# Kernel optimization log

Hardware: AMD Instinct MI355X
Metric: run time of the kernel (lower is better)

The kernel has to match this reference:

```python
import jax, jax.numpy as jnp
import numpy as np

N = 10000
E = 160000
D = 512
EPS = 1e-5


def _lin_params(key, out_d, in_d, bias=True):
    k1, k2 = jax.random.split(key)
    s = 1.0 / np.sqrt(in_d)
    W = jax.random.uniform(k1, (out_d, in_d), jnp.float32, -s, s)
    if bias:
        b = jax.random.uniform(k2, (out_d,), jnp.float32, -s, s)
        return W, b
    return (W,)


def setup_inputs() -> dict:
    key = jax.random.key(0)
    ks = jax.random.split(key, 16)
    inp = {
        "x": jax.random.normal(ks[0], (N, D), jnp.float32),
        "edge_index": jax.random.randint(ks[1], (2, E), 0, N, jnp.int64),
    }
    ki = 2
    for l in range(3):
        Wp, bp = _lin_params(ks[ki], D, D); ki += 1
        Wl, bl = _lin_params(ks[ki], D, D); ki += 1
        (Wr,) = _lin_params(ks[ki], D, D, bias=False); ki += 1
        inp[f"Wp{l}"] = Wp; inp[f"bp{l}"] = bp
        inp[f"Wl{l}"] = Wl; inp[f"bl{l}"] = bl
        inp[f"Wr{l}"] = Wr
        if l < 2:  # ReLU+LayerNorm between convs
            inp[f"g{l}"] = jnp.ones((D,), jnp.float32)
            inp[f"be{l}"] = jnp.zeros((D,), jnp.float32)
    return inp


def _sage_conv(x, src, dst, Wp, bp, Wl, bl, Wr):
    # PyG SAGEConv with project=True: project+ReLU messages, mean-aggregate, lin_l + lin_r(root)
    h = jax.nn.relu(x @ Wp.T + bp)                      # [N, D] projected messages
    agg = jax.ops.segment_sum(h[src], dst, num_segments=N)   # gather + scatter-add
    cnt = jax.ops.segment_sum(jnp.ones((src.shape[0],), x.dtype), dst, num_segments=N)
    agg = agg / jnp.maximum(cnt, 1.0)[:, None]          # mean over incoming edges
    return agg @ Wl.T + bl + x @ Wr.T


def _relu_ln(x, g, b):
    x = jax.nn.relu(x)
    mu = jnp.mean(x, axis=-1, keepdims=True)
    var = jnp.mean(jnp.square(x - mu), axis=-1, keepdims=True)
    return (x - mu) * jax.lax.rsqrt(var + EPS) * g + b


def reference(x, edge_index,
              Wp0, bp0, Wl0, bl0, Wr0, g0, be0,
              Wp1, bp1, Wl1, bl1, Wr1, g1, be1,
              Wp2, bp2, Wl2, bl2, Wr2):
    src, dst = edge_index[0], edge_index[1]
    x = _sage_conv(x, src, dst, Wp0, bp0, Wl0, bl0, Wr0)
    x = _relu_ln(x, g0, be0)
    x = _sage_conv(x, src, dst, Wp1, bp1, Wl1, bl1, Wr1)
    x = _relu_ln(x, g1, be1)
    x = _sage_conv(x, src, dst, Wp2, bp2, Wl2, bl2, Wr2)
    return x
```

## Files before the change

kernel.cpp:

```cpp
#include <hip/hip_runtime.h>
#include <cstdint>

#define D 512
#define TM 128
#define TN 64
#define BK 32
#define CAP 64

typedef unsigned short u16;
typedef __bf16 bf16x8 __attribute__((ext_vector_type(8)));
typedef float f32x4 __attribute__((ext_vector_type(4)));

__device__ __forceinline__ float bf2f(u16 u) {
    unsigned int x = ((unsigned int)u) << 16;
    return __builtin_bit_cast(float, x);
}
__device__ __forceinline__ u16 f2bf(float f) {
    unsigned int x = __builtin_bit_cast(unsigned int, f);
    x += 0x7fffu + ((x >> 16) & 1u);
    return (u16)(x >> 16);
}
__device__ __forceinline__ float loadf(const void* p, int i, bool bf) {
    return bf ? bf2f(((const u16*)p)[i]) : ((const float*)p)[i];
}
__device__ __forceinline__ void gload16(const u16* g, u16* l) {
    __builtin_amdgcn_global_load_lds(
        (const __attribute__((address_space(1))) void*)(uintptr_t)g,
        (__attribute__((address_space(3))) void*)(unsigned int)(uintptr_t)l,
        16, 0, 0);
}
__device__ __forceinline__ void drain_vm() {
    asm volatile("s_waitcnt vmcnt(0)" ::: "memory");
}
__device__ __forceinline__ bool is_bf16(const u16* xraw) {
    int lane = threadIdx.x & 63;
    u16 u = xraw[2 * lane];
    int e = (u >> 7) & 0xFF;
    unsigned long long b = __ballot(e >= 110 && e <= 129);
    return __popcll(b) >= 32;
}
__device__ __forceinline__ bool is_i64(const int* eraw) {
    int lane = threadIdx.x & 63;
    unsigned long long b = __ballot(eraw[2 * lane + 1] == 0);
    return __popcll(b) >= 32;
}

struct PrepArgs {
    const u16* xraw; const int* eraw;
    const void* W[9];
    const void* V[10];
    u16* xb; u16* Wb; float* vecf;
    int* cnt; u16* bucket;
    int M, E;
};

__global__ __launch_bounds__(256) void prep(PrepArgs a)
{
    const bool bf  = is_bf16(a.xraw);
    const bool i64 = is_i64(a.eraw);
    const int gt = blockIdx.x * 256 + threadIdx.x;
    const int gs = gridDim.x * 256;

    const int nx = a.M * D / 8;
    for (int i = gt; i < nx; i += gs) {
        if (bf) {
            *(uint4*)(a.xb + i * 8) = *(const uint4*)(a.xraw + i * 8);
        } else {
            const float* f = (const float*)a.xraw + i * 8;
            float4 p = *(const float4*)f, q = *(const float4*)(f + 4);
            u16 r[8] = {f2bf(p.x), f2bf(p.y), f2bf(p.z), f2bf(p.w),
                        f2bf(q.x), f2bf(q.y), f2bf(q.z), f2bf(q.w)};
            *(uint4*)(a.xb + i * 8) = *(uint4*)r;
        }
    }

    for (int i = gt; i < 9 * 32768; i += gs) {
        int m = i >> 15, j = i & 32767;
        const void* gsrc = nullptr;
        if (m == 3 || m == 5) gsrc = a.V[2];
        else if (m == 6 || m == 8) gsrc = a.V[6];
        const void* src = a.W[m];
        int c0 = (j * 8) & 511;
        float v[8];
        if (bf) {
            const u16* s = (const u16*)src + j * 8;
#pragma unroll
            for (int e = 0; e < 8; e++) v[e] = bf2f(s[e]);
        } else {
            const float* s = (const float*)src + j * 8;
#pragma unroll
            for (int e = 0; e < 8; e++) v[e] = s[e];
        }
        if (gsrc) {
#pragma unroll
            for (int e = 0; e < 8; e++) v[e] *= loadf(gsrc, c0 + e, bf);
        }
        u16 r[8];
#pragma unroll
        for (int e = 0; e < 8; e++) r[e] = f2bf(v[e]);
        *(uint4*)(a.Wb + (size_t)m * D * D + j * 8) = *(uint4*)r;
    }

    for (int e = gt; e < 10 * 512; e += gs) {
        int t = e >> 9, n = e & 511;
        float outv;
        if (t == 0)      outv = loadf(a.V[0], n, bf);
        else if (t == 1) outv = loadf(a.V[1], n, bf);
        else {
            int q = t - 2;
            const int wi[8] = {3, 3, 5, 5, 6, 6, 8, 8};
            const void* wraw = a.W[wi[q]];
            const void* dotv = (q < 4) ? ((q & 1) ? a.V[3] : a.V[2])
                                       : ((q & 1) ? a.V[7] : a.V[6]);
            float acc = 0.f;
            if (bf) {
                const u16* wr = (const u16*)wraw + (size_t)n * 512;
                for (int k = 0; k < 512; k++) acc += bf2f(wr[k]) * loadf(dotv, k, bf);
            } else {
                const float* wr = (const float*)wraw + (size_t)n * 512;
                for (int k = 0; k < 512; k++) acc += wr[k] * loadf(dotv, k, bf);
            }
            if (q & 1) {
                const void* braw = (q == 1) ? a.V[4] : (q == 3) ? a.V[5]
                                 : (q == 5) ? a.V[8] : a.V[9];
                acc += loadf(braw, n, bf);
            }
            outv = acc;
        }
        a.vecf[t * 512 + n] = outv;
    }

    for (int e2 = gt; e2 < a.E; e2 += gs) {
        int s, d;
        if (i64) { s = a.eraw[2 * e2]; d = a.eraw[2 * (a.E + e2)]; }
        else     { s = a.eraw[e2];     d = a.eraw[a.E + e2]; }
        s = min(max(s, 0), a.M - 1);
        d = min(max(d, 0), a.M - 1);
        int p = atomicAdd(&a.cnt[d], 1);
        if (p < CAP) a.bucket[(size_t)d * CAP + p] = (u16)s;
    }
}

template <bool LNIN>
__global__ __launch_bounds__(256) void gemm1k(
    const u16* __restrict__ A, const u16* __restrict__ W,
    const float* __restrict__ bias, const float* __restrict__ svec,
    const float* __restrict__ mu, const float* __restrict__ m2,
    u16* __restrict__ hout, int M)
{
    __shared__ __align__(16) u16 sA[2][TM * BK];
    __shared__ __align__(16) u16 sB[2][TN * BK];

    const int t    = threadIdx.x;
    const int m0   = blockIdx.x * TM;
    const int n0   = blockIdx.y * TN;
    const int wave = t >> 6, lane = t & 63;
    const int wm   = wave >> 1, wn = wave & 1;
    const int lrow = lane & 15, quad = lane >> 4;

    float rstd[4][4], nmu[4][4];
    if (LNIN) {
#pragma unroll
        for (int mi = 0; mi < 4; mi++)
#pragma unroll
            for (int r = 0; r < 4; r++) {
                int row = min(m0 + wm * 64 + mi * 16 + quad * 4 + r, M - 1);
                float mean = mu[row] * (1.f / 512.f);
                float var  = m2[row] * (1.f / 512.f) - mean * mean;
                float rs   = rsqrtf(fmaxf(var, 0.f) + 1e-5f);
                rstd[mi][r] = rs;
                nmu[mi][r]  = -mean * rs;
            }
    }

    f32x4 acc[4][2];
#pragma unroll
    for (int i = 0; i < 4; i++)
#pragma unroll
        for (int j = 0; j < 2; j++)
#pragma unroll
            for (int r = 0; r < 4; r++) acc[i][j][r] = 0.f;

    const int cA    = (t & 3) * 8;
    const int rowA0 = min(m0 + (t >> 2),      M - 1);
    const int rowA1 = min(m0 + 64 + (t >> 2), M - 1);
    const int rowB  = n0 + (t >> 2);
    const u16* gA0 = A + (size_t)rowA0 * D + cA;
    const u16* gA1 = A + (size_t)rowA1 * D + cA;
    const u16* gB  = W + (size_t)rowB  * D + cA;

    gload16(gA0, &sA[0][(size_t)t * 8]);
    gload16(gA1, &sA[0][(size_t)(t + 256) * 8]);
    gload16(gB,  &sB[0][(size_t)t * 8]);

#pragma unroll 1
    for (int k0 = 0; k0 < D; k0 += BK) {
        const int it  = k0 >> 5;
        const int cur = it & 1, nxt = cur ^ 1;
        drain_vm();
        __syncthreads();
        const int k1 = k0 + BK;
        if (k1 < D) {
            gload16(gA0 + k1, &sA[nxt][(size_t)t * 8]);
            gload16(gA1 + k1, &sA[nxt][(size_t)(t + 256) * 8]);
            gload16(gB  + k1, &sB[nxt][(size_t)t * 8]);
        }
        bf16x8 af[4], bfr[2];
#pragma unroll
        for (int mi = 0; mi < 4; mi++)
            af[mi] = *(const bf16x8*)&sA[cur][(wm * 64 + mi * 16 + lrow) * BK + quad * 8];
#pragma unroll
        for (int ni = 0; ni < 2; ni++)
            bfr[ni] = *(const bf16x8*)&sB[cur][(wn * 32 + ni * 16 + lrow) * BK + quad * 8];
#pragma unroll
        for (int mi = 0; mi < 4; mi++)
#pragma unroll
            for (int ni = 0; ni < 2; ni++)
                acc[mi][ni] = __builtin_amdgcn_mfma_f32_16x16x32_bf16(
                    af[mi], bfr[ni], acc[mi][ni], 0, 0, 0);
    }

#pragma unroll
    for (int ni = 0; ni < 2; ni++) {
        int col = n0 + wn * 32 + ni * 16 + lrow;
        float bv = bias[col];
        float sv = LNIN ? svec[col] : 0.f;
#pragma unroll
        for (int mi = 0; mi < 4; mi++) {
            int row0 = m0 + wm * 64 + mi * 16 + quad * 4;
#pragma unroll
            for (int r = 0; r < 4; r++) {
                int row = row0 + r;
                if (row < M) {
                    float v = LNIN ? rstd[mi][r] * acc[mi][ni][r] + nmu[mi][r] * sv + bv
                                   : acc[mi][ni][r] + bv;
                    hout[(size_t)row * D + col] = f2bf(fmaxf(v, 0.f));
                }
            }
        }
    }
}

template <bool LNIN, bool STATS, bool FINAL>
__global__ __launch_bounds__(256) void gemm2k(
    const u16* __restrict__ A0, const u16* __restrict__ W0,
    const u16* __restrict__ A1, const u16* __restrict__ W1,
    const float* __restrict__ bias, const float* __restrict__ s2vec,
    const float* __restrict__ mu_in, const float* __restrict__ m2_in,
    float* __restrict__ mu_out, float* __restrict__ m2_out,
    void* __restrict__ out, const u16* __restrict__ xraw, int M)
{
    __shared__ __align__(16) u16 sA[2][TM * BK];
    __shared__ __align__(16) u16 sB[2][TN * BK];

    const int t    = threadIdx.x;
    const int m0   = blockIdx.x * TM;
    const int n0   = blockIdx.y * TN;
    const int wave = t >> 6, lane = t & 63;
    const int wm   = wave >> 1, wn = wave & 1;
    const int lrow = lane & 15, quad = lane >> 4;

    const bool out_bf16 = FINAL ? is_bf16(xraw) : true;

    float rstd[4][4], nmu[4][4], inv[4][4];
    if (LNIN) {
#pragma unroll
        for (int mi = 0; mi < 4; mi++)
#pragma unroll
            for (int r = 0; r < 4; r++) {
                int row = min(m0 + wm * 64 + mi * 16 + quad * 4 + r, M - 1);
                float mean = mu_in[row] * (1.f / 512.f);
                float var  = m2_in[row] * (1.f / 512.f) - mean * mean;
                float s    = sqrtf(fmaxf(var, 0.f) + 1e-5f);
                float rs   = 1.f / s;
                rstd[mi][r] = rs;
                inv[mi][r]  = s;
                nmu[mi][r]  = -mean * rs;
            }
    }

    f32x4 acc[4][2];
#pragma unroll
    for (int i = 0; i < 4; i++)
#pragma unroll
        for (int j = 0; j < 2; j++)
#pragma unroll
            for (int r = 0; r < 4; r++) acc[i][j][r] = 0.f;

    const int cA    = (t & 3) * 8;
    const int rowA0 = min(m0 + (t >> 2),      M - 1);
    const int rowA1 = min(m0 + 64 + (t >> 2), M - 1);
    const int rowB  = n0 + (t >> 2);

    gload16(A0 + (size_t)rowA0 * D + cA, &sA[0][(size_t)t * 8]);
    gload16(A0 + (size_t)rowA1 * D + cA, &sA[0][(size_t)(t + 256) * 8]);
    gload16(W0 + (size_t)rowB  * D + cA, &sB[0][(size_t)t * 8]);

#pragma unroll 1
    for (int kk = 0; kk < 2 * D; kk += BK) {
        const int it  = kk >> 5;
        const int cur = it & 1, nxt = cur ^ 1;
        drain_vm();
        __syncthreads();
        const int kn = kk + BK;
        if (kn < 2 * D) {
            const u16* A = (kn >= D) ? A1 : A0;
            const u16* W = (kn >= D) ? W1 : W0;
            const int k = kn & (D - 1);
            gload16(A + (size_t)rowA0 * D + k + cA, &sA[nxt][(size_t)t * 8]);
            gload16(A + (size_t)rowA1 * D + k + cA, &sA[nxt][(size_t)(t + 256) * 8]);
            gload16(W + (size_t)rowB  * D + k + cA, &sB[nxt][(size_t)t * 8]);
        }
        if (LNIN && kk == D) {
#pragma unroll
            for (int mi = 0; mi < 4; mi++)
#pragma unroll
                for (int ni = 0; ni < 2; ni++)
#pragma unroll
                    for (int r = 0; r < 4; r++) acc[mi][ni][r] *= inv[mi][r];
        }
        bf16x8 af[4], bfr[2];
#pragma unroll
        for (int mi = 0; mi < 4; mi++)
            af[mi] = *(const bf16x8*)&sA[cur][(wm * 64 + mi * 16 + lrow) * BK + quad * 8];
#pragma unroll
        for (int ni = 0; ni < 2; ni++)
            bfr[ni] = *(const bf16x8*)&sB[cur][(wn * 32 + ni * 16 + lrow) * BK + quad * 8];
#pragma unroll
        for (int mi = 0; mi < 4; mi++)
#pragma unroll
            for (int ni = 0; ni < 2; ni++)
                acc[mi][ni] = __builtin_amdgcn_mfma_f32_16x16x32_bf16(
                    af[mi], bfr[ni], acc[mi][ni], 0, 0, 0);
    }

    float bvv[2], svv[2];
#pragma unroll
    for (int ni = 0; ni < 2; ni++) {
        int col = n0 + wn * 32 + ni * 16 + lrow;
        bvv[ni] = bias[col];
        svv[ni] = LNIN ? s2vec[col] : 0.f;
    }

#pragma unroll
    for (int mi = 0; mi < 4; mi++) {
#pragma unroll
        for (int r = 0; r < 4; r++) {
            int row = m0 + wm * 64 + mi * 16 + quad * 4 + r;
            float sr = 0.f, s2r = 0.f;
#pragma unroll
            for (int ni = 0; ni < 2; ni++) {
                int col = n0 + wn * 32 + ni * 16 + lrow;
                float v = acc[mi][ni][r];
                if (LNIN) v = rstd[mi][r] * v + nmu[mi][r] * svv[ni] + bvv[ni];
                else      v += bvv[ni];
                if (FINAL) {
                    if (row < M) {
                        if (out_bf16) ((u16*)out)[(size_t)row * D + col] = f2bf(v);
                        else          ((float*)out)[(size_t)row * D + col] = v;
                    }
                } else {
                    u16 zb = f2bf(fmaxf(v, 0.f));
                    float z = bf2f(zb);
                    if (row < M) ((u16*)out)[(size_t)row * D + col] = zb;
                    sr  += z;
                    s2r += z * z;
                }
            }
            if (STATS) {
#pragma unroll
                for (int off = 1; off <= 8; off <<= 1) {
                    sr  += __shfl_xor(sr, off);
                    s2r += __shfl_xor(s2r, off);
                }
                if (lrow == 0 && row < M) {
                    atomicAdd(&mu_out[row], sr);
                    atomicAdd(&m2_out[row], s2r);
                }
            }
        }
    }
}

__global__ __launch_bounds__(256) void aggregate(
    const u16* __restrict__ h, const int* __restrict__ cnt,
    const u16* __restrict__ bucket, u16* __restrict__ agg, int M)
{
    const int w = threadIdx.x >> 6, lane = threadIdx.x & 63;
    const int n = blockIdx.x * 4 + w;

    __shared__ u16 sidx[4][CAP];
    int deg = 0, dd = 0;
    if (n < M) {
        deg = cnt[n];
        dd  = min(deg, CAP);
        if (lane < dd) sidx[w][lane] = bucket[(size_t)n * CAP + lane];
    }
    __syncthreads();
    if (n >= M) return;

    float a[8] = {0.f, 0.f, 0.f, 0.f, 0.f, 0.f, 0.f, 0.f};
    int i = 0;
    for (; i + 4 <= dd; i += 4) {
        uint4 v0 = *(const uint4*)(h + (size_t)sidx[w][i]     * D + lane * 8);
        uint4 v1 = *(const uint4*)(h + (size_t)sidx[w][i + 1] * D + lane * 8);
        uint4 v2 = *(const uint4*)(h + (size_t)sidx[w][i + 2] * D + lane * 8);
        uint4 v3 = *(const uint4*)(h + (size_t)sidx[w][i + 3] * D + lane * 8);
        const unsigned int* u0 = (const unsigned int*)&v0;
        const unsigned int* u1 = (const unsigned int*)&v1;
        const unsigned int* u2 = (const unsigned int*)&v2;
        const unsigned int* u3 = (const unsigned int*)&v3;
#pragma unroll
        for (int j = 0; j < 4; j++) {
            a[2 * j]     += bf2f((u16)(u0[j] & 0xffffu)) + bf2f((u16)(u1[j] & 0xffffu))
                          + bf2f((u16)(u2[j] & 0xffffu)) + bf2f((u16)(u3[j] & 0xffffu));
            a[2 * j + 1] += bf2f((u16)(u0[j] >> 16)) + bf2f((u16)(u1[j] >> 16))
                          + bf2f((u16)(u2[j] >> 16)) + bf2f((u16)(u3[j] >> 16));
        }
    }
    for (; i < dd; i++) {
        uint4 v0 = *(const uint4*)(h + (size_t)sidx[w][i] * D + lane * 8);
        const unsigned int* u0 = (const unsigned int*)&v0;
#pragma unroll
        for (int j = 0; j < 4; j++) {
            a[2 * j]     += bf2f((u16)(u0[j] & 0xffffu));
            a[2 * j + 1] += bf2f((u16)(u0[j] >> 16));
        }
    }

    float invd = 1.f / fmaxf((float)deg, 1.f);
    u16 r[8];
#pragma unroll
    for (int j = 0; j < 8; j++) r[j] = f2bf(a[j] * invd);
    *(uint4*)(agg + (size_t)n * D + lane * 8) = *(uint4*)r;
}

extern "C" void kernel_launch(void* const* d_in, const int* in_sizes, int n_in,
                              void* d_out, int out_size, void* d_ws, size_t ws_size,
                              hipStream_t stream)
{
    const int M = in_sizes[0] / D;
    const int E = in_sizes[1] / 2;

    PrepArgs a;
    a.xraw = (const u16*)d_in[0];
    a.eraw = (const int*)d_in[1];
    {
        int idx = 2;
        for (int l = 0; l < 3; l++) {
            a.W[l * 3 + 0] = d_in[idx++];
            a.V[l * 4 + 0] = d_in[idx++];
            a.W[l * 3 + 1] = d_in[idx++];
            a.V[l * 4 + 1] = d_in[idx++];
            a.W[l * 3 + 2] = d_in[idx++];
            if (l < 2) {
                a.V[l * 4 + 2] = d_in[idx++];
                a.V[l * 4 + 3] = d_in[idx++];
            }
        }
    }

    char* w = (char*)d_ws;
    auto alloc = [&](size_t bytes) { void* p = w; w += (bytes + 255) & ~(size_t)255; return p; };
    u16*   xb   = (u16*)  alloc((size_t)M * D * 2);
    u16*   h    = (u16*)  alloc((size_t)M * D * 2);
    u16*   aggb = (u16*)  alloc((size_t)M * D * 2);
    u16*   z0   = (u16*)  alloc((size_t)M * D * 2);
    u16*   z1   = (u16*)  alloc((size_t)M * D * 2);
    u16*   Wb   = (u16*)  alloc((size_t)9 * D * D * 2);
    float* vecf = (float*)alloc((size_t)10 * 512 * 4);
    int*   cnt  = (int*)  alloc((size_t)M * 4);
    float* mu0  = (float*)alloc((size_t)M * 4);
    float* m20  = (float*)alloc((size_t)M * 4);
    float* mu1  = (float*)alloc((size_t)M * 4);
    float* m21  = (float*)alloc((size_t)M * 4);
    u16* bucket = (u16*)  alloc((size_t)M * CAP * 2);

    a.xb = xb; a.Wb = Wb; a.vecf = vecf; a.cnt = cnt; a.bucket = bucket;
    a.M = M; a.E = E;

    hipMemsetAsync(cnt, 0, (size_t)((char*)bucket - (char*)cnt), stream);
    prep<<<dim3(1024), dim3(256), 0, stream>>>(a);

    const size_t DD = (size_t)D * D;
    dim3 gg((M + TM - 1) / TM, D / TN);
    dim3 ga((M + 3) / 4);

    gemm1k<false><<<gg, dim3(256), 0, stream>>>(
        xb, Wb + 0 * DD, vecf + 0 * 512, nullptr, nullptr, nullptr, h, M);
    aggregate<<<ga, dim3(256), 0, stream>>>(h, cnt, bucket, aggb, M);
    gemm2k<false, true, false><<<gg, dim3(256), 0, stream>>>(
        aggb, Wb + 1 * DD, xb, Wb + 2 * DD, vecf + 1 * 512, nullptr,
        nullptr, nullptr, mu0, m20, z0, a.xraw, M);

    gemm1k<true><<<gg, dim3(256), 0, stream>>>(
        z0, Wb + 3 * DD, vecf + 3 * 512, vecf + 2 * 512, mu0, m20, h, M);
    aggregate<<<ga, dim3(256), 0, stream>>>(h, cnt, bucket, aggb, M);
    gemm2k<true, true, false><<<gg, dim3(256), 0, stream>>>(
        aggb, Wb + 4 * DD, z0, Wb + 5 * DD, vecf + 5 * 512, vecf + 4 * 512,
        mu0, m20, mu1, m21, z1, a.xraw, M);

    gemm1k<true><<<gg, dim3(256), 0, stream>>>(
        z1, Wb + 6 * DD, vecf + 7 * 512, vecf + 6 * 512, mu1, m21, h, M);
    aggregate<<<ga, dim3(256), 0, stream>>>(h, cnt, bucket, aggb, M);
    gemm2k<true, false, true><<<gg, dim3(256), 0, stream>>>(
        aggb, Wb + 7 * DD, z1, Wb + 8 * DD, vecf + 9 * 512, vecf + 8 * 512,
        mu1, m21, nullptr, nullptr, d_out, a.xraw, M);
}
```

Before: 365.2 us.

## Parallelize prep bias-folding dot products per wave and remap GEMM tiles XCD-aware

```diff
diff --git a/kernel.cpp b/kernel.cpp
--- a/kernel.cpp
+++ b/kernel.cpp
@@ -43,6 +43,14 @@
     int lane = threadIdx.x & 63;
     unsigned long long b = __ballot(eraw[2 * lane + 1] == 0);
     return __popcll(b) >= 32;
+}
+
+__device__ __forceinline__ void tile_map(int blk, int km, int M, int& m0, int& n0, bool& valid) {
+    const int r = blk & 7, j = blk >> 3;
+    const int mt = r + 8 * (j % km);
+    const int nt = j / km;
+    m0 = mt * TM; n0 = nt * TN;
+    valid = (m0 < M);
 }
 
 struct PrepArgs {
@@ -60,6 +68,7 @@
     const bool i64 = is_i64(a.eraw);
     const int gt = blockIdx.x * 256 + threadIdx.x;
     const int gs = gridDim.x * 256;
+    const int lane = threadIdx.x & 63;
 
     const int nx = a.M * D / 8;
     for (int i = gt; i < nx; i += gs) {
@@ -101,33 +110,41 @@
         *(uint4*)(a.Wb + (size_t)m * D * D + j * 8) = *(uint4*)r;
     }
 
-    for (int e = gt; e < 10 * 512; e += gs) {
-        int t = e >> 9, n = e & 511;
-        float outv;
-        if (t == 0)      outv = loadf(a.V[0], n, bf);
-        else if (t == 1) outv = loadf(a.V[1], n, bf);
-        else {
-            int q = t - 2;
+    if (gt < 1024) {
+        int t = gt >> 9, n = gt & 511;
+        a.vecf[t * 512 + n] = loadf(a.V[t], n, bf);
+    }
+
+    {
+        const int gw = blockIdx.x * 4 + (threadIdx.x >> 6);
+        if (gw < 4096) {
+            const int q = gw >> 9, n = gw & 511;
             const int wi[8] = {3, 3, 5, 5, 6, 6, 8, 8};
             const void* wraw = a.W[wi[q]];
             const void* dotv = (q < 4) ? ((q & 1) ? a.V[3] : a.V[2])
                                        : ((q & 1) ? a.V[7] : a.V[6]);
             float acc = 0.f;
+            const int k0 = lane * 8;
             if (bf) {
-                const u16* wr = (const u16*)wraw + (size_t)n * 512;
-                for (int k = 0; k < 512; k++) acc += bf2f(wr[k]) * loadf(dotv, k, bf);
+                const u16* wr = (const u16*)wraw + (size_t)n * 512 + k0;
+#pragma unroll
+                for (int e = 0; e < 8; e++) acc += bf2f(wr[e]) * loadf(dotv, k0 + e, bf);
             } else {
-                const float* wr = (const float*)wraw + (size_t)n * 512;
-                for (int k = 0; k < 512; k++) acc += wr[k] * loadf(dotv, k, bf);
-            }
-            if (q & 1) {
-                const void* braw = (q == 1) ? a.V[4] : (q == 3) ? a.V[5]
-                                 : (q == 5) ? a.V[8] : a.V[9];
-                acc += loadf(braw, n, bf);
-            }
-            outv = acc;
-        }
-        a.vecf[t * 512 + n] = outv;
+                const float* wr = (const float*)wraw + (size_t)n * 512 + k0;
+#pragma unroll
+                for (int e = 0; e < 8; e++) acc += wr[e] * loadf(dotv, k0 + e, bf);
+            }
+#pragma unroll
+            for (int off = 32; off >= 1; off >>= 1) acc += __shfl_xor(acc, off);
+            if (lane == 0) {
+                if (q & 1) {
+                    const void* braw = (q == 1) ? a.V[4] : (q == 3) ? a.V[5]
+                                     : (q == 5) ? a.V[8] : a.V[9];
+                    acc += loadf(braw, n, bf);
+                }
+                a.vecf[(q + 2) * 512 + n] = acc;
+            }
+        }
     }
 
     for (int e2 = gt; e2 < a.E; e2 += gs) {
@@ -151,9 +168,11 @@
     __shared__ __align__(16) u16 sA[2][TM * BK];
     __shared__ __align__(16) u16 sB[2][TN * BK];
 
+    int m0, n0; bool valid;
+    tile_map(blockIdx.x, gridDim.x >> 6, M, m0, n0, valid);
+    if (!valid) return;
+
     const int t    = threadIdx.x;
-    const int m0   = blockIdx.x * TM;
-    const int n0   = blockIdx.y * TN;
     const int wave = t >> 6, lane = t & 63;
     const int wm   = wave >> 1, wn = wave & 1;
     const int lrow = lane & 15, quad = lane >> 4;
@@ -253,9 +272,11 @@
     __shared__ __align__(16) u16 sA[2][TM * BK];
     __shared__ __align__(16) u16 sB[2][TN * BK];
 
+    int m0, n0; bool valid;
+    tile_map(blockIdx.x, gridDim.x >> 6, M, m0, n0, valid);
+    if (!valid) return;
+
     const int t    = threadIdx.x;
-    const int m0   = blockIdx.x * TM;
-    const int n0   = blockIdx.y * TN;
     const int wave = t >> 6, lane = t & 63;
     const int wm   = wave >> 1, wn = wave & 1;
     const int lrow = lane & 15, quad = lane >> 4;
@@ -483,7 +504,9 @@
     prep<<<dim3(1024), dim3(256), 0, stream>>>(a);
 
     const size_t DD = (size_t)D * D;
-    dim3 gg((M + TM - 1) / TM, D / TN);
+    const int MT = (M + TM - 1) / TM;
+    const int NB = ((MT + 7) / 8) * 8 * (D / TN);
+    dim3 gg(NB);
     dim3 ga((M + 3) / 4);
 
     gemm1k<false><<<gg, dim3(256), 0, stream>>>(
```

Result: faster. 311.7 us (-14.6%).
